# Optimization experiments

Measured on AMD Instinct MI355X. Metric: run time of the kernel, lower is better.

The kernel has to match this reference:

```python
import jax, jax.numpy as jnp
import numpy as np

N, E = 50000, 400000
IN_DIM, HID, OUT = 512, 256, 128


def _lin(key, fan_in, fan_out, bias=True):
    k1, k2 = jax.random.split(key)
    s = 1.0 / np.sqrt(fan_in)
    W = jax.random.uniform(k1, (fan_in, fan_out), minval=-s, maxval=s, dtype=jnp.float32)
    if bias:
        b = jax.random.uniform(k2, (fan_out,), minval=-s, maxval=s, dtype=jnp.float32)
        return W, b
    return W


def setup_inputs() -> dict:
    key = jax.random.key(0)
    ks = jax.random.split(key, 16)
    feature_data = jax.random.normal(ks[0], (N, IN_DIM), dtype=jnp.float32)
    edge_info = jax.random.randint(ks[1], (2, E), 0, N, dtype=jnp.int32)
    W1, b1 = _lin(ks[2], IN_DIM, HID)
    W2, b2 = _lin(ks[3], HID, HID)
    W3, b3 = _lin(ks[4], HID, HID)
    # SAGEConv params: lin_l (aggregated neighbors, with bias), lin_r (root, no bias)
    Wl1, bl1 = _lin(ks[5], HID, HID); Wr1 = _lin(ks[6], HID, HID, bias=False)
    WlH, blH = _lin(ks[7], HID, HID); WrH = _lin(ks[8], HID, HID, bias=False)
    Wl2, bl2 = _lin(ks[9], HID, HID); Wr2 = _lin(ks[10], HID, HID, bias=False)
    Wp1, bp1 = _lin(ks[11], HID, HID)
    Wp2, bp2 = _lin(ks[12], HID, HID)
    Wp3, bp3 = _lin(ks[13], HID, OUT)
    return dict(feature_data=feature_data, edge_info=edge_info,
                W1=W1, b1=b1, W2=W2, b2=b2, W3=W3, b3=b3,
                Wl1=Wl1, bl1=bl1, Wr1=Wr1,
                WlH=WlH, blH=blH, WrH=WrH,
                Wl2=Wl2, bl2=bl2, Wr2=Wr2,
                Wp1=Wp1, bp1=bp1, Wp2=Wp2, bp2=bp2, Wp3=Wp3, bp3=bp3)


def _sage_softmax_conv(x, src, dst, Wl, bl, Wr, n_nodes):
    # messages are source node features
    m = x[src]                                                   # [E, d]
    mx = jax.ops.segment_max(m, dst, num_segments=n_nodes)      # per-dest, per-channel max
    e = jnp.exp(m - mx[dst])                                     # stable softmax numerator
    s = jax.ops.segment_sum(e, dst, num_segments=n_nodes)
    alpha = e / s[dst]                                           # per-dest channel softmax
    aggr = jax.ops.segment_sum(alpha * m, dst, num_segments=n_nodes)  # [N, d]
    return aggr @ Wl + bl + x @ Wr


def reference(feature_data, edge_info,
              W1, b1, W2, b2, W3, b3,
              Wl1, bl1, Wr1, WlH, blH, WrH, Wl2, bl2, Wr2,
              Wp1, bp1, Wp2, bp2, Wp3, bp3):
    n = feature_data.shape[0]
    src, dst = edge_info[0], edge_info[1]
    # eval mode: dropout is identity
    x = jax.nn.relu(feature_data @ W1 + b1)
    x = jax.nn.relu(x @ W2 + b2)
    x = jax.nn.relu(x @ W3 + b3)
    x = jax.nn.relu(_sage_softmax_conv(x, src, dst, Wl1, bl1, Wr1, n))
    x = jax.nn.relu(_sage_softmax_conv(x, src, dst, WlH, blH, WrH, n))
    x = jax.nn.relu(_sage_softmax_conv(x, src, dst, Wl2, bl2, Wr2, n))
    x = jax.nn.relu(x @ Wp1 + bp1)
    x = jax.nn.relu(x @ Wp2 + bp2)
    return jnp.tanh(x @ Wp3 + bp3)
```

## Files before the change

kernel.cpp:

```cpp
#include <hip/hip_runtime.h>
#include <hip/hip_bf16.h>
#include <math.h>

typedef short s8v __attribute__((ext_vector_type(8)));
typedef float f32x4 __attribute__((ext_vector_type(4)));
typedef unsigned u32x4 __attribute__((ext_vector_type(4)));

__device__ __forceinline__ ushort f2bf(float f) {
    __hip_bfloat16 h = __float2bfloat16(f);
    return *reinterpret_cast<ushort*>(&h);
}
__device__ __forceinline__ float bf2f(ushort u) {
    return __uint_as_float(((unsigned)u) << 16);
}
__device__ __forceinline__ unsigned pack_split(float v) {
    ushort h = f2bf(v);
    ushort l = f2bf(v - bf2f(h));
    return ((unsigned)h << 16) | (unsigned)l;
}
__device__ __forceinline__ float unpack_f(unsigned p) {
    return __uint_as_float(p & 0xffff0000u) + __uint_as_float(p << 16);
}
__device__ __forceinline__ void gload16(const void* g, void* l) {
    __builtin_amdgcn_global_load_lds(
        (const __attribute__((address_space(1))) void*)g,
        (__attribute__((address_space(3))) void*)l, 16, 0, 0);
}
__device__ __forceinline__ unsigned lds_addr(const void* p) {
    return (unsigned)(size_t)(const __attribute__((address_space(3))) void*)p;
}
__device__ __forceinline__ void unpack8(const u32x4 p0, const u32x4 p1, s8v& hi, s8v& lo) {
    union { s8v v; unsigned u[4]; } H, L;
    H.u[0] = (p0[0] >> 16) | (p0[1] & 0xffff0000u);
    H.u[1] = (p0[2] >> 16) | (p0[3] & 0xffff0000u);
    H.u[2] = (p1[0] >> 16) | (p1[1] & 0xffff0000u);
    H.u[3] = (p1[2] >> 16) | (p1[3] & 0xffff0000u);
    L.u[0] = (p0[0] & 0xffffu) | (p0[1] << 16);
    L.u[1] = (p0[2] & 0xffffu) | (p0[3] << 16);
    L.u[2] = (p1[0] & 0xffffu) | (p1[1] << 16);
    L.u[3] = (p1[2] & 0xffffu) | (p1[3] << 16);
    hi = H.v; lo = L.v;
}
__device__ __forceinline__ void cvt8(const u32x4 p0, const u32x4 p1, s8v& hi, s8v& lo) {
    union { s8v v; ushort e[8]; } H, L;
    float f[8] = {__uint_as_float(p0[0]), __uint_as_float(p0[1]),
                  __uint_as_float(p0[2]), __uint_as_float(p0[3]),
                  __uint_as_float(p1[0]), __uint_as_float(p1[1]),
                  __uint_as_float(p1[2]), __uint_as_float(p1[3])};
    #pragma unroll
    for (int e = 0; e < 8; ++e) {
        ushort h = f2bf(f[e]);
        H.e[e] = (ushort)h;
        L.e[e] = f2bf(f[e] - bf2f(h));
    }
    hi = H.v; lo = L.v;
}
template<bool AF32>
__device__ __forceinline__ void frag_a(const u32x4 p0, const u32x4 p1, s8v& hi, s8v& lo) {
    if constexpr (AF32) cvt8(p0, p1, hi, lo);
    else                unpack8(p0, p1, hi, lo);
}

#define DSR(dst, addr, OFF) \
    asm volatile("ds_read_b128 %0, %1 offset:" #OFF : "=v"(dst) : "v"(addr))

#define TRI(ah, al, bh, bl, C) \
    C = __builtin_amdgcn_mfma_f32_16x16x32_bf16(ah, bh, C, 0, 0, 0); \
    C = __builtin_amdgcn_mfma_f32_16x16x32_bf16(ah, bl, C, 0, 0, 0); \
    C = __builtin_amdgcn_mfma_f32_16x16x32_bf16(al, bh, C, 0, 0, 0);


__global__ __launch_bounds__(256)
void hist_kernel(const int* __restrict__ dst, int* __restrict__ cnt, int E) {
    int e = blockIdx.x * 256 + threadIdx.x;
    if (e < E) atomicAdd(&cnt[dst[e]], 1);
}

__global__ __launch_bounds__(256)
void scan_part(const int* __restrict__ cnt, int* __restrict__ bsum, int n) {
    __shared__ int s[256];
    int b = blockIdx.x, t = threadIdx.x;
    int i0 = b * 1024 + t * 4;
    int v = 0;
    if (i0 + 3 < n) {
        int4 q = *(const int4*)(cnt + i0);
        v = q.x + q.y + q.z + q.w;
    } else {
        for (int i = 0; i < 4; ++i) if (i0 + i < n) v += cnt[i0 + i];
    }
    s[t] = v;
    __syncthreads();
    for (int d = 128; d > 0; d >>= 1) {
        if (t < d) s[t] += s[t + d];
        __syncthreads();
    }
    if (t == 0) bsum[b] = s[0];
}

__global__ __launch_bounds__(64)
void scan_top(int* __restrict__ bsum, int nb) {
    int l = threadIdx.x;
    int own = (l < nb) ? bsum[l] : 0;
    int v = own;
    #pragma unroll
    for (int d = 1; d < 64; d <<= 1) {
        int u = __shfl_up(v, d, 64);
        if (l >= d) v += u;
    }
    if (l < nb) bsum[l] = v - own;
}

__global__ __launch_bounds__(256)
void scan_final(const int* __restrict__ cnt, const int* __restrict__ bsum,
                int* __restrict__ off, int n, int E) {
    __shared__ int s[256];
    int b = blockIdx.x, t = threadIdx.x;
    int i0 = b * 1024 + t * 4;
    int v0 = 0, v1 = 0, v2 = 0, v3 = 0;
    if (i0 + 3 < n) {
        int4 q = *(const int4*)(cnt + i0);
        v0 = q.x; v1 = q.y; v2 = q.z; v3 = q.w;
    } else {
        if (i0     < n) v0 = cnt[i0];
        if (i0 + 1 < n) v1 = cnt[i0 + 1];
        if (i0 + 2 < n) v2 = cnt[i0 + 2];
        if (i0 + 3 < n) v3 = cnt[i0 + 3];
    }
    int tsum = v0 + v1 + v2 + v3;
    s[t] = tsum;
    __syncthreads();
    for (int d = 1; d < 256; d <<= 1) {
        int u = (t >= d) ? s[t - d] : 0;
        __syncthreads();
        s[t] += u;
        __syncthreads();
    }
    int excl = s[t] - tsum + bsum[b];
    if (i0     < n) off[i0]     = excl;
    if (i0 + 1 < n) off[i0 + 1] = excl + v0;
    if (i0 + 2 < n) off[i0 + 2] = excl + v0 + v1;
    if (i0 + 3 < n) off[i0 + 3] = excl + v0 + v1 + v2;
    if (b == 0 && t == 0) off[n] = E;
}

__global__ __launch_bounds__(256)
void scatter_kernel(const int* __restrict__ src, const int* __restrict__ dst,
                    int* __restrict__ cur, const int* __restrict__ off,
                    int* __restrict__ csr, int E) {
    int e = blockIdx.x * 256 + threadIdx.x;
    if (e < E) {
        int d = dst[e];
        int pos = off[d] + atomicAdd(&cur[d], 1);
        csr[pos] = src[e];
    }
}


struct PrepW {
    const float* W[12];
    unsigned* D[12];
    int end[12];
    int stride[12];
    int koff[12];
    int nshift[12];
};

__global__ __launch_bounds__(256)
void prep_weights(PrepW a, int total) {
    int id = blockIdx.x * 256 + threadIdx.x;
    if (id >= total) return;
    int s = 0;
    #pragma unroll
    for (int i = 0; i < 12; ++i) if (id >= a.end[i]) s = i + 1;
    int base = (s == 0) ? 0 : a.end[s - 1];
    int e = id - base;
    int Nmask = (1 << a.nshift[s]) - 1;
    int n = e & Nmask;
    int k = e >> a.nshift[s];
    float w = a.W[s][(size_t)k * (Nmask + 1) + n];
    a.D[s][(size_t)n * a.stride[s] + a.koff[s] + k] = pack_split(w);
}


__global__ __launch_bounds__(256)
void sage_aggr_pk(const unsigned* __restrict__ X, const int* __restrict__ csr,
                  const int* __restrict__ off, unsigned* __restrict__ O, int nN) {
    int node = blockIdx.x * 4 + (threadIdx.x >> 6);
    if (node >= nN) return;
    int c4 = (threadIdx.x & 63) * 4;
    int s0 = off[node], s1 = off[node + 1];
    float m0 = -INFINITY, m1 = -INFINITY, m2 = -INFINITY, m3 = -INFINITY;
    float se0 = 0, se1 = 0, se2 = 0, se3 = 0;
    float sm0 = 0, sm1 = 0, sm2 = 0, sm3 = 0;
#define ONLSTEP(vv, mm, ss, pp) { float nm = fmaxf(mm, vv); float r = __expf(mm - nm); \
    float p = __expf(vv - nm); ss = ss * r + p; pp = pp * r + p * (vv); mm = nm; }
    for (int j = s0; j < s1; ++j) {
        uint4 p = *(const uint4*)(X + (size_t)csr[j] * 256 + c4);
        float v0 = unpack_f(p.x), v1 = unpack_f(p.y), v2 = unpack_f(p.z), v3 = unpack_f(p.w);
        ONLSTEP(v0, m0, se0, sm0) ONLSTEP(v1, m1, se1, sm1)
        ONLSTEP(v2, m2, se2, sm2) ONLSTEP(v3, m3, se3, sm3)
    }
#undef ONLSTEP
    uint4 o;
    o.x = pack_split((s1 > s0) ? sm0 / se0 : 0.f);
    o.y = pack_split((s1 > s0) ? sm1 / se1 : 0.f);
    o.z = pack_split((s1 > s0) ? sm2 / se2 : 0.f);
    o.w = pack_split((s1 > s0) ? sm3 / se3 : 0.f);
    *(uint4*)(O + (size_t)node * 256 + c4) = o;
}


template<int NT1, int NT2, bool AF32, int NB, bool DOTANH>
__global__ __launch_bounds__(512, 2)
void gemm_pipe(const float* __restrict__ A1f, const unsigned* __restrict__ A1,
               const unsigned* __restrict__ A2,
               const unsigned* __restrict__ B,
               const float* __restrict__ bias,
               unsigned* __restrict__ Cpk, float* __restrict__ Cf, int M) {
    constexpr int NT = NT1 + NT2;
    constexpr int KU = NT * 32;
    __shared__ unsigned lds[3][12288];

    const int tid = threadIdx.x;
    const int l = tid & 63;
    const int w = tid >> 6;
    const int wm = w >> 2, wn = w & 3;
    const int li = l & 15, kq = l >> 4;
    const int bm = blockIdx.x * 128;

    const int srow = 8 * w + (l >> 3);
    const int schunk = (l & 7) ^ (l >> 3);

    const unsigned lbase = lds_addr(&lds[0][0]);
    const unsigned swz0 = (unsigned)((((2 * kq)) ^ (li & 7)) * 16);
    const unsigned aoff = (unsigned)((wm * 64 + li) * 128) + swz0;
    const unsigned boff = 16384u + (unsigned)((wn * 64 + li) * 128) + swz0;

    f32x4 acc[4][4];
    #pragma unroll
    for (int i = 0; i < 4; ++i)
        #pragma unroll
        for (int j = 0; j < 4; ++j) acc[i][j] = (f32x4){0.f, 0.f, 0.f, 0.f};

    auto STAGE = [&](int t, int buf) {
        #pragma unroll
        for (int s = 0; s < 2; ++s) {
            int r = 64 * s + srow;
            int gr = bm + r; gr = (gr < M) ? gr : (M - 1);
            const void* src;
            if constexpr (AF32) {
                src = A1f + (size_t)gr * KU + t * 32 + schunk * 4;
            } else if constexpr (NT2 > 0) {
                src = (t < NT1) ? (const void*)(A1 + (size_t)gr * (NT1 * 32) + t * 32 + schunk * 4)
                                : (const void*)(A2 + (size_t)gr * (NT2 * 32) + (t - NT1) * 32 + schunk * 4);
            } else {
                src = A1 + (size_t)gr * KU + t * 32 + schunk * 4;
            }
            gload16(src, &lds[buf][s * 2048 + w * 256 + l * 4]);
        }
        #pragma unroll
        for (int s = 0; s < 4; ++s) {
            int n = 64 * s + srow;
            int gn = (n < NB) ? n : (NB - 1);
            const unsigned* src = B + (size_t)gn * KU + t * 32 + schunk * 4;
            gload16(src, &lds[buf][4096 + s * 2048 + w * 256 + l * 4]);
        }
    };

    STAGE(0, 0);
    STAGE(1, 1);

    #pragma unroll
    for (int t = 0; t < NT; ++t) {
        if (t + 1 < NT) asm volatile("s_waitcnt vmcnt(6)" ::: "memory");
        else            asm volatile("s_waitcnt vmcnt(0)" ::: "memory");
        __builtin_amdgcn_s_barrier();

        const int buf = t % 3;
        const unsigned lb = lbase + (unsigned)buf * 49152u;
        unsigned ab = lb + aoff, bb = lb + boff;
        unsigned ab1 = ab ^ 16u, bb1 = bb ^ 16u;

        u32x4 B0, B1, B2, B3, B4, B5, B6, B7;
        u32x4 A0, A4, A1v, A5, A2v, A6, A3, A7;
        DSR(B0, bb, 0);    DSR(B1, bb, 2048);  DSR(B2, bb, 4096);  DSR(B3, bb, 6144);
        DSR(B4, bb1, 0);   DSR(B5, bb1, 2048); DSR(B6, bb1, 4096); DSR(B7, bb1, 6144);
        DSR(A0, ab, 0);    DSR(A4, ab1, 0);
        __builtin_amdgcn_sched_barrier(0);

        if (t + 2 < NT) STAGE(t + 2, (t + 2) % 3);
        __builtin_amdgcn_sched_barrier(0);

        DSR(A1v, ab, 2048); DSR(A5, ab1, 2048);
        asm volatile("s_waitcnt lgkmcnt(2)" ::: "memory");
        __builtin_amdgcn_sched_barrier(0);

        s8v bh0, bl0, bh1, bl1, bh2, bl2, bh3, bl3;
        unpack8(B0, B4, bh0, bl0);
        unpack8(B1, B5, bh1, bl1);
        unpack8(B2, B6, bh2, bl2);
        unpack8(B3, B7, bh3, bl3);

        __builtin_amdgcn_s_setprio(1);
        {
            s8v ah, al;
            frag_a<AF32>(A0, A4, ah, al);
            TRI(ah, al, bh0, bl0, acc[0][0]) TRI(ah, al, bh1, bl1, acc[0][1])
            TRI(ah, al, bh2, bl2, acc[0][2]) TRI(ah, al, bh3, bl3, acc[0][3])
        }
        __builtin_amdgcn_sched_barrier(0);
        DSR(A2v, ab, 4096); DSR(A6, ab1, 4096);
        asm volatile("s_waitcnt lgkmcnt(2)" ::: "memory");
        __builtin_amdgcn_sched_barrier(0);
        {
            s8v ah, al;
            frag_a<AF32>(A1v, A5, ah, al);
            TRI(ah, al, bh0, bl0, acc[1][0]) TRI(ah, al, bh1, bl1, acc[1][1])
            TRI(ah, al, bh2, bl2, acc[1][2]) TRI(ah, al, bh3, bl3, acc[1][3])
        }
        __builtin_amdgcn_sched_barrier(0);
        DSR(A3, ab, 6144); DSR(A7, ab1, 6144);
        asm volatile("s_waitcnt lgkmcnt(2)" ::: "memory");
        __builtin_amdgcn_sched_barrier(0);
        {
            s8v ah, al;
            frag_a<AF32>(A2v, A6, ah, al);
            TRI(ah, al, bh0, bl0, acc[2][0]) TRI(ah, al, bh1, bl1, acc[2][1])
            TRI(ah, al, bh2, bl2, acc[2][2]) TRI(ah, al, bh3, bl3, acc[2][3])
        }
        asm volatile("s_waitcnt lgkmcnt(0)" ::: "memory");
        __builtin_amdgcn_sched_barrier(0);
        {
            s8v ah, al;
            frag_a<AF32>(A3, A7, ah, al);
            TRI(ah, al, bh0, bl0, acc[3][0]) TRI(ah, al, bh1, bl1, acc[3][1])
            TRI(ah, al, bh2, bl2, acc[3][2]) TRI(ah, al, bh3, bl3, acc[3][3])
        }
        __builtin_amdgcn_s_setprio(0);
    }

    #pragma unroll
    for (int j = 0; j < 4; ++j) {
        int col = wn * 64 + 16 * j + li;
        float b = bias[(col < NB) ? col : 0];
        #pragma unroll
        for (int i = 0; i < 4; ++i) {
            int row0 = bm + wm * 64 + 16 * i + kq * 4;
            #pragma unroll
            for (int r = 0; r < 4; ++r) {
                float v = acc[i][j][r] + b;
                if constexpr (DOTANH) {
                    if (row0 + r < M && col < NB)
                        Cf[(size_t)(row0 + r) * NB + col] = tanhf(v);
                } else {
                    Cpk[(size_t)(row0 + r) * 256 + col] = pack_split(fmaxf(v, 0.f));
                }
            }
        }
    }
}


extern "C" void kernel_launch(void* const* d_in, const int* in_sizes, int n_in,
                              void* d_out, int out_size, void* d_ws, size_t ws_size,
                              hipStream_t stream) {
    const float* feat = (const float*)d_in[0];
    const int* einfo = (const int*)d_in[1];
    const float* b1 = (const float*)d_in[3];
    const float* b2 = (const float*)d_in[5];
    const float* b3 = (const float*)d_in[7];
    const float* bl1 = (const float*)d_in[9];
    const float* blH = (const float*)d_in[12];
    const float* bl2 = (const float*)d_in[15];
    const float* bp1 = (const float*)d_in[18];
    const float* bp2 = (const float*)d_in[20];
    const float* bp3 = (const float*)d_in[22];

    const int IN_DIM = 512;
    const int N = in_sizes[0] / IN_DIM;
    const int E = in_sizes[1] / 2;
    const int* src = einfo;
    const int* dst = einfo + E;
    const int M_pad = ((N + 127) / 128) * 128;
    const size_t PLANE_U = (size_t)M_pad * 256;

    unsigned* P0 = (unsigned*)d_ws;
    unsigned* P1 = P0 + PLANE_U;
    unsigned* P2 = P1 + PLANE_U;
    unsigned* wp = P2 + PLANE_U;

    const int gsz[9] = {131072, 65536, 65536, 131072, 131072, 131072, 65536, 65536, 32768};
    unsigned* G[9];
    {
        unsigned* c = wp;
        for (int i = 0; i < 9; ++i) { G[i] = c; c += gsz[i]; }
        wp = c;
    }

    const int widx[12]   = {2, 4, 6, 8, 10, 11, 13, 14, 16, 17, 19, 21};
    const int wplane[12] = {0, 1, 2, 3, 3, 4, 4, 5, 5, 6, 7, 8};
    const int wstr[12]   = {512, 256, 256, 512, 512, 512, 512, 512, 512, 256, 256, 256};
    const int wkoff[12]  = {0, 0, 0, 0, 256, 0, 256, 0, 256, 0, 0, 0};
    const int wnsh[12]   = {8, 8, 8, 8, 8, 8, 8, 8, 8, 8, 8, 7};
    const int welem[12]  = {131072, 65536, 65536, 65536, 65536, 65536, 65536,
                            65536, 65536, 65536, 65536, 32768};

    PrepW pa;
    int acc_end = 0;
    for (int i = 0; i < 12; ++i) {
        pa.W[i] = (const float*)d_in[widx[i]];
        pa.D[i] = G[wplane[i]];
        pa.stride[i] = wstr[i];
        pa.koff[i] = wkoff[i];
        pa.nshift[i] = wnsh[i];
        acc_end += welem[i];
        pa.end[i] = acc_end;
    }

    int* ioff = (int*)wp;
    int* icnt = ioff + ((N + 1 + 3) & ~3);
    int* icur = icnt + ((N + 3) & ~3);
    int* csr  = icur + ((N + 3) & ~3);
    int* bsum = csr + ((E + 3) & ~3);

    const int NBLK = (N + 1023) / 1024;

    hipMemsetAsync(icnt, 0, (size_t)N * sizeof(int), stream);
    hipMemsetAsync(icur, 0, (size_t)N * sizeof(int), stream);
    hist_kernel<<<(E + 255) / 256, 256, 0, stream>>>(dst, icnt, E);
    scan_part<<<NBLK, 256, 0, stream>>>(icnt, bsum, N);
    scan_top<<<1, 64, 0, stream>>>(bsum, NBLK);
    scan_final<<<NBLK, 256, 0, stream>>>(icnt, bsum, ioff, N, E);
    scatter_kernel<<<(E + 255) / 256, 256, 0, stream>>>(src, dst, icur, ioff, csr, E);
    prep_weights<<<(acc_end + 255) / 256, 256, 0, stream>>>(pa, acc_end);

    const int GB = M_pad / 128;
    const int GA = (N + 3) / 4;

    gemm_pipe<16, 0, true, 256, false><<<GB, 512, 0, stream>>>(
        feat, nullptr, nullptr, G[0], b1, P0, nullptr, N);
    gemm_pipe<8, 0, false, 256, false><<<GB, 512, 0, stream>>>(
        nullptr, P0, nullptr, G[1], b2, P1, nullptr, N);
    gemm_pipe<8, 0, false, 256, false><<<GB, 512, 0, stream>>>(
        nullptr, P1, nullptr, G[2], b3, P0, nullptr, N);

    sage_aggr_pk<<<GA, 256, 0, stream>>>(P0, csr, ioff, P1, N);
    gemm_pipe<8, 8, false, 256, false><<<GB, 512, 0, stream>>>(
        nullptr, P1, P0, G[3], bl1, P2, nullptr, N);

    sage_aggr_pk<<<GA, 256, 0, stream>>>(P2, csr, ioff, P1, N);
    gemm_pipe<8, 8, false, 256, false><<<GB, 512, 0, stream>>>(
        nullptr, P1, P2, G[4], blH, P0, nullptr, N);

    sage_aggr_pk<<<GA, 256, 0, stream>>>(P0, csr, ioff, P1, N);
    gemm_pipe<8, 8, false, 256, false><<<GB, 512, 0, stream>>>(
        nullptr, P1, P0, G[5], bl2, P2, nullptr, N);

    gemm_pipe<8, 0, false, 256, false><<<GB, 512, 0, stream>>>(
        nullptr, P2, nullptr, G[6], bp1, P0, nullptr, N);
    gemm_pipe<8, 0, false, 256, false><<<GB, 512, 0, stream>>>(
        nullptr, P0, nullptr, G[7], bp2, P1, nullptr, N);
    gemm_pipe<8, 0, false, 128, true><<<GB, 512, 0, stream>>>(
        nullptr, P1, nullptr, G[8], bp3, nullptr, (float*)d_out, N);
}
```

Before: 652.1 us.

## Store split-bf16 activations and weights as separate hi/lo planes, drop online max

Replaces the packed hi|lo 32-bit split-bf16 format with two separate bf16 planes for activations and weights. The GEMM can then read MFMA fragments straight from LDS without per-iteration unpack shuffles, which also changes the LDS staging layout and swizzle. The aggregation kernel drops the online-softmax running max and instead clamps inputs to 60 before exp. That is safe only because inputs are post-ReLU and bounded, but it risks overflow or precision loss for large values. Aggregation now reads two separate 8-byte loads per edge instead of one 16-byte load.

```diff
diff --git a/kernel.cpp b/kernel.cpp
--- a/kernel.cpp
+++ b/kernel.cpp
@@ -12,14 +12,6 @@
 }
 __device__ __forceinline__ float bf2f(ushort u) {
     return __uint_as_float(((unsigned)u) << 16);
-}
-__device__ __forceinline__ unsigned pack_split(float v) {
-    ushort h = f2bf(v);
-    ushort l = f2bf(v - bf2f(h));
-    return ((unsigned)h << 16) | (unsigned)l;
-}
-__device__ __forceinline__ float unpack_f(unsigned p) {
-    return __uint_as_float(p & 0xffff0000u) + __uint_as_float(p << 16);
 }
 __device__ __forceinline__ void gload16(const void* g, void* l) {
     __builtin_amdgcn_global_load_lds(
@@ -28,18 +20,6 @@
 }
 __device__ __forceinline__ unsigned lds_addr(const void* p) {
     return (unsigned)(size_t)(const __attribute__((address_space(3))) void*)p;
-}
-__device__ __forceinline__ void unpack8(const u32x4 p0, const u32x4 p1, s8v& hi, s8v& lo) {
-    union { s8v v; unsigned u[4]; } H, L;
-    H.u[0] = (p0[0] >> 16) | (p0[1] & 0xffff0000u);
-    H.u[1] = (p0[2] >> 16) | (p0[3] & 0xffff0000u);
-    H.u[2] = (p1[0] >> 16) | (p1[1] & 0xffff0000u);
-    H.u[3] = (p1[2] >> 16) | (p1[3] & 0xffff0000u);
-    L.u[0] = (p0[0] & 0xffffu) | (p0[1] << 16);
-    L.u[1] = (p0[2] & 0xffffu) | (p0[3] << 16);
-    L.u[2] = (p1[0] & 0xffffu) | (p1[1] << 16);
-    L.u[3] = (p1[2] & 0xffffu) | (p1[3] << 16);
-    hi = H.v; lo = L.v;
 }
 __device__ __forceinline__ void cvt8(const u32x4 p0, const u32x4 p1, s8v& hi, s8v& lo) {
     union { s8v v; ushort e[8]; } H, L;
@@ -54,11 +34,6 @@
         L.e[e] = f2bf(f[e] - bf2f(h));
     }
     hi = H.v; lo = L.v;
-}
-template<bool AF32>
-__device__ __forceinline__ void frag_a(const u32x4 p0, const u32x4 p1, s8v& hi, s8v& lo) {
-    if constexpr (AF32) cvt8(p0, p1, hi, lo);
-    else                unpack8(p0, p1, hi, lo);
 }
 
 #define DSR(dst, addr, OFF) \
@@ -158,7 +133,8 @@
 
 struct PrepW {
     const float* W[12];
-    unsigned* D[12];
+    ushort* H[12];
+    ushort* L[12];
     int end[12];
     int stride[12];
     int koff[12];
@@ -178,48 +154,67 @@
     int n = e & Nmask;
     int k = e >> a.nshift[s];
     float w = a.W[s][(size_t)k * (Nmask + 1) + n];
-    a.D[s][(size_t)n * a.stride[s] + a.koff[s] + k] = pack_split(w);
-}
-
-
-__global__ __launch_bounds__(256)
-void sage_aggr_pk(const unsigned* __restrict__ X, const int* __restrict__ csr,
-                  const int* __restrict__ off, unsigned* __restrict__ O, int nN) {
+    ushort hi = f2bf(w);
+    size_t idx = (size_t)n * a.stride[s] + a.koff[s] + k;
+    a.H[s][idx] = hi;
+    a.L[s][idx] = f2bf(w - bf2f(hi));
+}
+
+
+__global__ __launch_bounds__(256)
+void sage_aggr(const ushort* __restrict__ XH, const ushort* __restrict__ XL,
+               const int* __restrict__ csr, const int* __restrict__ off,
+               ushort* __restrict__ OH, ushort* __restrict__ OL, int nN) {
     int node = blockIdx.x * 4 + (threadIdx.x >> 6);
     if (node >= nN) return;
     int c4 = (threadIdx.x & 63) * 4;
     int s0 = off[node], s1 = off[node + 1];
-    float m0 = -INFINITY, m1 = -INFINITY, m2 = -INFINITY, m3 = -INFINITY;
     float se0 = 0, se1 = 0, se2 = 0, se3 = 0;
     float sm0 = 0, sm1 = 0, sm2 = 0, sm3 = 0;
-#define ONLSTEP(vv, mm, ss, pp) { float nm = fmaxf(mm, vv); float r = __expf(mm - nm); \
-    float p = __expf(vv - nm); ss = ss * r + p; pp = pp * r + p * (vv); mm = nm; }
     for (int j = s0; j < s1; ++j) {
-        uint4 p = *(const uint4*)(X + (size_t)csr[j] * 256 + c4);
-        float v0 = unpack_f(p.x), v1 = unpack_f(p.y), v2 = unpack_f(p.z), v3 = unpack_f(p.w);
-        ONLSTEP(v0, m0, se0, sm0) ONLSTEP(v1, m1, se1, sm1)
-        ONLSTEP(v2, m2, se2, sm2) ONLSTEP(v3, m3, se3, sm3)
-    }
-#undef ONLSTEP
-    uint4 o;
-    o.x = pack_split((s1 > s0) ? sm0 / se0 : 0.f);
-    o.y = pack_split((s1 > s0) ? sm1 / se1 : 0.f);
-    o.z = pack_split((s1 > s0) ? sm2 / se2 : 0.f);
-    o.w = pack_split((s1 > s0) ? sm3 / se3 : 0.f);
-    *(uint4*)(O + (size_t)node * 256 + c4) = o;
+        size_t b = (size_t)csr[j] * 256 + c4;
+        ushort4 h = *(const ushort4*)(XH + b);
+        ushort4 l = *(const ushort4*)(XL + b);
+        float v0 = bf2f(h.x) + bf2f(l.x);
+        float v1 = bf2f(h.y) + bf2f(l.y);
+        float v2 = bf2f(h.z) + bf2f(l.z);
+        float v3 = bf2f(h.w) + bf2f(l.w);
+        float e0 = __expf(fminf(v0, 60.f));
+        float e1 = __expf(fminf(v1, 60.f));
+        float e2 = __expf(fminf(v2, 60.f));
+        float e3 = __expf(fminf(v3, 60.f));
+        se0 += e0; sm0 = fmaf(v0, e0, sm0);
+        se1 += e1; sm1 = fmaf(v1, e1, sm1);
+        se2 += e2; sm2 = fmaf(v2, e2, sm2);
+        se3 += e3; sm3 = fmaf(v3, e3, sm3);
+    }
+    float o0 = (s1 > s0) ? sm0 / se0 : 0.f;
+    float o1 = (s1 > s0) ? sm1 / se1 : 0.f;
+    float o2 = (s1 > s0) ? sm2 / se2 : 0.f;
+    float o3 = (s1 > s0) ? sm3 / se3 : 0.f;
+    ushort4 oh, ol;
+    oh.x = f2bf(o0); ol.x = f2bf(o0 - bf2f(oh.x));
+    oh.y = f2bf(o1); ol.y = f2bf(o1 - bf2f(oh.y));
+    oh.z = f2bf(o2); ol.z = f2bf(o2 - bf2f(oh.z));
+    oh.w = f2bf(o3); ol.w = f2bf(o3 - bf2f(oh.w));
+    size_t ob = (size_t)node * 256 + c4;
+    *(ushort4*)(OH + ob) = oh;
+    *(ushort4*)(OL + ob) = ol;
 }
 
 
 template<int NT1, int NT2, bool AF32, int NB, bool DOTANH>
 __global__ __launch_bounds__(512, 2)
-void gemm_pipe(const float* __restrict__ A1f, const unsigned* __restrict__ A1,
-               const unsigned* __restrict__ A2,
-               const unsigned* __restrict__ B,
+void gemm_pipe(const float* __restrict__ Af,
+               const ushort* __restrict__ A1H, const ushort* __restrict__ A1L,
+               const ushort* __restrict__ A2H, const ushort* __restrict__ A2L,
+               const ushort* __restrict__ BH, const ushort* __restrict__ BL,
                const float* __restrict__ bias,
-               unsigned* __restrict__ Cpk, float* __restrict__ Cf, int M) {
+               ushort* __restrict__ CH, ushort* __restrict__ CL,
+               float* __restrict__ Cf, int M) {
     constexpr int NT = NT1 + NT2;
     constexpr int KU = NT * 32;
-    __shared__ unsigned lds[3][12288];
+    __shared__ ushort lds[3][24576];
 
     const int tid = threadIdx.x;
     const int l = tid & 63;
@@ -228,13 +223,15 @@
     const int li = l & 15, kq = l >> 4;
     const int bm = blockIdx.x * 128;
 
-    const int srow = 8 * w + (l >> 3);
-    const int schunk = (l & 7) ^ (l >> 3);
+    const int arow = 16 * w + (l >> 2);
+    const int achk = (l & 3) ^ ((l >> 2) & 3);
+    const int frow = 8 * w + (l >> 3);
+    const int fchk = (l & 7) ^ ((l >> 3) & 7);
 
     const unsigned lbase = lds_addr(&lds[0][0]);
-    const unsigned swz0 = (unsigned)((((2 * kq)) ^ (li & 7)) * 16);
-    const unsigned aoff = (unsigned)((wm * 64 + li) * 128) + swz0;
-    const unsigned boff = 16384u + (unsigned)((wn * 64 + li) * 128) + swz0;
+    const unsigned aoffA = (unsigned)((wm * 64 + li) * 64 + ((kq ^ (li & 3)) * 16));
+    const unsigned boffB = 16384u + (unsigned)((wn * 64 + li) * 64 + ((kq ^ (li & 3)) * 16));
+    const unsigned aoffF = (unsigned)((wm * 64 + li) * 128 + (((2 * kq) ^ (li & 7)) * 16));
 
     f32x4 acc[4][4];
     #pragma unroll
@@ -243,27 +240,31 @@
         for (int j = 0; j < 4; ++j) acc[i][j] = (f32x4){0.f, 0.f, 0.f, 0.f};
 
     auto STAGE = [&](int t, int buf) {
+        if constexpr (AF32) {
+            #pragma unroll
+            for (int s = 0; s < 2; ++s) {
+                int gr = bm + 64 * s + frow; gr = (gr < M) ? gr : (M - 1);
+                const float* src = Af + (size_t)gr * KU + t * 32 + fchk * 4;
+                gload16(src, &lds[buf][(64 * s + 8 * w) * 64 + l * 8]);
+            }
+        } else {
+            int gr = bm + arow; gr = (gr < M) ? gr : (M - 1);
+            const ushort *pH, *pL; int tt, KA;
+            if constexpr (NT2 > 0) {
+                if (t >= NT1) { pH = A2H; pL = A2L; tt = t - NT1; KA = NT2 * 32; }
+                else          { pH = A1H; pL = A1L; tt = t;       KA = NT1 * 32; }
+            } else { pH = A1H; pL = A1L; tt = t; KA = KU; }
+            size_t ab = (size_t)gr * KA + tt * 32 + achk * 8;
+            gload16(pH + ab, &lds[buf][512 * w + 8 * l]);
+            gload16(pL + ab, &lds[buf][4096 + 512 * w + 8 * l]);
+        }
         #pragma unroll
         for (int s = 0; s < 2; ++s) {
-            int r = 64 * s + srow;
-            int gr = bm + r; gr = (gr < M) ? gr : (M - 1);
-            const void* src;
-            if constexpr (AF32) {
-                src = A1f + (size_t)gr * KU + t * 32 + schunk * 4;
-            } else if constexpr (NT2 > 0) {
-                src = (t < NT1) ? (const void*)(A1 + (size_t)gr * (NT1 * 32) + t * 32 + schunk * 4)
-                                : (const void*)(A2 + (size_t)gr * (NT2 * 32) + (t - NT1) * 32 + schunk * 4);
-            } else {
-                src = A1 + (size_t)gr * KU + t * 32 + schunk * 4;
-            }
-            gload16(src, &lds[buf][s * 2048 + w * 256 + l * 4]);
-        }
-        #pragma unroll
-        for (int s = 0; s < 4; ++s) {
-            int n = 64 * s + srow;
+            int n = 32 * w + 16 * s + (l >> 2);
             int gn = (n < NB) ? n : (NB - 1);
-            const unsigned* src = B + (size_t)gn * KU + t * 32 + schunk * 4;
-            gload16(src, &lds[buf][4096 + s * 2048 + w * 256 + l * 4]);
+            size_t bb = (size_t)gn * KU + t * 32 + achk * 8;
+            gload16(BH + bb, &lds[buf][8192  + 1024 * w + 512 * s + 8 * l]);
+            gload16(BL + bb, &lds[buf][16384 + 1024 * w + 512 * s + 8 * l]);
         }
     };
 
@@ -278,65 +279,87 @@
 
         const int buf = t % 3;
         const unsigned lb = lbase + (unsigned)buf * 49152u;
-        unsigned ab = lb + aoff, bb = lb + boff;
-        unsigned ab1 = ab ^ 16u, bb1 = bb ^ 16u;
-
-        u32x4 B0, B1, B2, B3, B4, B5, B6, B7;
-        u32x4 A0, A4, A1v, A5, A2v, A6, A3, A7;
-        DSR(B0, bb, 0);    DSR(B1, bb, 2048);  DSR(B2, bb, 4096);  DSR(B3, bb, 6144);
-        DSR(B4, bb1, 0);   DSR(B5, bb1, 2048); DSR(B6, bb1, 4096); DSR(B7, bb1, 6144);
-        DSR(A0, ab, 0);    DSR(A4, ab1, 0);
-        __builtin_amdgcn_sched_barrier(0);
-
-        if (t + 2 < NT) STAGE(t + 2, (t + 2) % 3);
-        __builtin_amdgcn_sched_barrier(0);
-
-        DSR(A1v, ab, 2048); DSR(A5, ab1, 2048);
-        asm volatile("s_waitcnt lgkmcnt(2)" ::: "memory");
-        __builtin_amdgcn_sched_barrier(0);
-
-        s8v bh0, bl0, bh1, bl1, bh2, bl2, bh3, bl3;
-        unpack8(B0, B4, bh0, bl0);
-        unpack8(B1, B5, bh1, bl1);
-        unpack8(B2, B6, bh2, bl2);
-        unpack8(B3, B7, bh3, bl3);
-
-        __builtin_amdgcn_s_setprio(1);
-        {
-            s8v ah, al;
-            frag_a<AF32>(A0, A4, ah, al);
-            TRI(ah, al, bh0, bl0, acc[0][0]) TRI(ah, al, bh1, bl1, acc[0][1])
-            TRI(ah, al, bh2, bl2, acc[0][2]) TRI(ah, al, bh3, bl3, acc[0][3])
+
+        s8v BH0, BH1, BH2, BH3, BL0, BL1, BL2, BL3;
+        if constexpr (AF32) {
+            unsigned bh_b = lb + boffB, bl_b = bh_b + 16384u;
+            unsigned ab = lb + aoffF, ab1 = ab ^ 16u;
+            u32x4 F0, F1, F2, F3, F4, F5, F6, F7;
+            DSR(BH0, bh_b, 0); DSR(BH1, bh_b, 1024); DSR(BH2, bh_b, 2048); DSR(BH3, bh_b, 3072);
+            DSR(BL0, bl_b, 0); DSR(BL1, bl_b, 1024); DSR(BL2, bl_b, 2048); DSR(BL3, bl_b, 3072);
+            DSR(F0, ab, 0); DSR(F4, ab1, 0);
+            __builtin_amdgcn_sched_barrier(0);
+            if (t + 2 < NT) STAGE(t + 2, (t + 2) % 3);
+            __builtin_amdgcn_sched_barrier(0);
+            DSR(F1, ab, 2048); DSR(F5, ab1, 2048);
+            asm volatile("s_waitcnt lgkmcnt(2)" ::: "memory");
+            __builtin_amdgcn_sched_barrier(0);
+            __builtin_amdgcn_s_setprio(1);
+            {
+                s8v ah, al; cvt8(F0, F4, ah, al);
+                TRI(ah, al, BH0, BL0, acc[0][0]) TRI(ah, al, BH1, BL1, acc[0][1])
+                TRI(ah, al, BH2, BL2, acc[0][2]) TRI(ah, al, BH3, BL3, acc[0][3])
+            }
+            __builtin_amdgcn_sched_barrier(0);
+            DSR(F2, ab, 4096); DSR(F6, ab1, 4096);
+            asm volatile("s_waitcnt lgkmcnt(2)" ::: "memory");
+            __builtin_amdgcn_sched_barrier(0);
+            {
+                s8v ah, al; cvt8(F1, F5, ah, al);
+                TRI(ah, al, BH0, BL0, acc[1][0]) TRI(ah, al, BH1, BL1, acc[1][1])
+                TRI(ah, al, BH2, BL2, acc[1][2]) TRI(ah, al, BH3, BL3, acc[1][3])
+            }
+            __builtin_amdgcn_sched_barrier(0);
+            DSR(F3, ab, 6144); DSR(F7, ab1, 6144);
+            asm volatile("s_waitcnt lgkmcnt(2)" ::: "memory");
+            __builtin_amdgcn_sched_barrier(0);
+            {
+                s8v ah, al; cvt8(F2, F6, ah, al);
+                TRI(ah, al, BH0, BL0, acc[2][0]) TRI(ah, al, BH1, BL1, acc[2][1])
+                TRI(ah, al, BH2, BL2, acc[2][2]) TRI(ah, al, BH3, BL3, acc[2][3])
+            }
+            asm volatile("s_waitcnt lgkmcnt(0)" ::: "memory");
+            __builtin_amdgcn_sched_barrier(0);
+            {
+                s8v ah, al; cvt8(F3, F7, ah, al);
+                TRI(ah, al, BH0, BL0, acc[3][0]) TRI(ah, al, BH1, BL1, acc[3][1])
+                TRI(ah, al, BH2, BL2, acc[3][2]) TRI(ah, al, BH3, BL3, acc[3][3])
+            }
+            __builtin_amdgcn_s_setprio(0);
+        } else {
+            unsigned ah_b = lb + aoffA, al_b = ah_b + 8192u;
+            unsigned bh_b = lb + boffB, bl_b = bh_b + 16384u;
+            s8v AH0, AH1, AH2, AH3, AL0, AL1, AL2, AL3;
+            DSR(BH0, bh_b, 0); DSR(BH1, bh_b, 1024); DSR(BH2, bh_b, 2048); DSR(BH3, bh_b, 3072);
+            DSR(BL0, bl_b, 0); DSR(BL1, bl_b, 1024); DSR(BL2, bl_b, 2048); DSR(BL3, bl_b, 3072);
+            DSR(AH0, ah_b, 0); DSR(AL0, al_b, 0);
+            __builtin_amdgcn_sched_barrier(0);
+            if (t + 2 < NT) STAGE(t + 2, (t + 2) % 3);
+            __builtin_amdgcn_sched_barrier(0);
+            DSR(AH1, ah_b, 1024); DSR(AL1, al_b, 1024);
+            asm volatile("s_waitcnt lgkmcnt(2)" ::: "memory");
+            __builtin_amdgcn_sched_barrier(0);
+            __builtin_amdgcn_s_setprio(1);
+            TRI(AH0, AL0, BH0, BL0, acc[0][0]) TRI(AH0, AL0, BH1, BL1, acc[0][1])
+            TRI(AH0, AL0, BH2, BL2, acc[0][2]) TRI(AH0, AL0, BH3, BL3, acc[0][3])
+            __builtin_amdgcn_sched_barrier(0);
+            DSR(AH2, ah_b, 2048); DSR(AL2, al_b, 2048);
+            asm volatile("s_waitcnt lgkmcnt(2)" ::: "memory");
+            __builtin_amdgcn_sched_barrier(0);
+            TRI(AH1, AL1, BH0, BL0, acc[1][0]) TRI(AH1, AL1, BH1, BL1, acc[1][1])
+            TRI(AH1, AL1, BH2, BL2, acc[1][2]) TRI(AH1, AL1, BH3, BL3, acc[1][3])
+            __builtin_amdgcn_sched_barrier(0);
+            DSR(AH3, ah_b, 3072); DSR(AL3, al_b, 3072);
+            asm volatile("s_waitcnt lgkmcnt(2)" ::: "memory");
+            __builtin_amdgcn_sched_barrier(0);
+            TRI(AH2, AL2, BH0, BL0, acc[2][0]) TRI(AH2, AL2, BH1, BL1, acc[2][1])
+            TRI(AH2, AL2, BH2, BL2, acc[2][2]) TRI(AH2, AL2, BH3, BL3, acc[2][3])
+            asm volatile("s_waitcnt lgkmcnt(0)" ::: "memory");
+            __builtin_amdgcn_sched_barrier(0);
+            TRI(AH3, AL3, BH0, BL0, acc[3][0]) TRI(AH3, AL3, BH1, BL1, acc[3][1])
+            TRI(AH3, AL3, BH2, BL2, acc[3][2]) TRI(AH3, AL3, BH3, BL3, acc[3][3])
+            __builtin_amdgcn_s_setprio(0);
         }
-        __builtin_amdgcn_sched_barrier(0);
-        DSR(A2v, ab, 4096); DSR(A6, ab1, 4096);
-        asm volatile("s_waitcnt lgkmcnt(2)" ::: "memory");
-        __builtin_amdgcn_sched_barrier(0);
-        {
-            s8v ah, al;
-            frag_a<AF32>(A1v, A5, ah, al);
-            TRI(ah, al, bh0, bl0, acc[1][0]) TRI(ah, al, bh1, bl1, acc[1][1])
-            TRI(ah, al, bh2, bl2, acc[1][2]) TRI(ah, al, bh3, bl3, acc[1][3])
-        }
-        __builtin_amdgcn_sched_barrier(0);
-        DSR(A3, ab, 6144); DSR(A7, ab1, 6144);
-        asm volatile("s_waitcnt lgkmcnt(2)" ::: "memory");
-        __builtin_amdgcn_sched_barrier(0);
-        {
-            s8v ah, al;
-            frag_a<AF32>(A2v, A6, ah, al);
-            TRI(ah, al, bh0, bl0, acc[2][0]) TRI(ah, al, bh1, bl1, acc[2][1])
-            TRI(ah, al, bh2, bl2, acc[2][2]) TRI(ah, al, bh3, bl3, acc[2][3])
-        }
-        asm volatile("s_waitcnt lgkmcnt(0)" ::: "memory");
-        __builtin_amdgcn_sched_barrier(0);
-        {
-            s8v ah, al;
-            frag_a<AF32>(A3, A7, ah, al);
-            TRI(ah, al, bh0, bl0, acc[3][0]) TRI(ah, al, bh1, bl1, acc[3][1])
-            TRI(ah, al, bh2, bl2, acc[3][2]) TRI(ah, al, bh3, bl3, acc[3][3])
-        }
-        __builtin_amdgcn_s_setprio(0);
     }
 
     #pragma unroll
@@ -353,7 +376,11 @@
                     if (row0 + r < M && col < NB)
                         Cf[(size_t)(row0 + r) * NB + col] = tanhf(v);
                 } else {
-                    Cpk[(size_t)(row0 + r) * 256 + col] = pack_split(fmaxf(v, 0.f));
+                    v = fmaxf(v, 0.f);
+                    ushort h = f2bf(v);
+                    size_t idx = (size_t)(row0 + r) * 256 + col;
+                    CH[idx] = h;
+                    CL[idx] = f2bf(v - bf2f(h));
                 }
             }
         }
@@ -382,20 +409,16 @@
     const int* src = einfo;
     const int* dst = einfo + E;
     const int M_pad = ((N + 127) / 128) * 128;
-    const size_t PLANE_U = (size_t)M_pad * 256;
-
-    unsigned* P0 = (unsigned*)d_ws;
-    unsigned* P1 = P0 + PLANE_U;
-    unsigned* P2 = P1 + PLANE_U;
-    unsigned* wp = P2 + PLANE_U;
+    const size_t PL = (size_t)M_pad * 256;
+
+    ushort* W = (ushort*)d_ws;
+    ushort* P0H = W; W += PL;  ushort* P0L = W; W += PL;
+    ushort* P1H = W; W += PL;  ushort* P1L = W; W += PL;
+    ushort* P2H = W; W += PL;  ushort* P2L = W; W += PL;
 
     const int gsz[9] = {131072, 65536, 65536, 131072, 131072, 131072, 65536, 65536, 32768};
-    unsigned* G[9];
-    {
-        unsigned* c = wp;
-        for (int i = 0; i < 9; ++i) { G[i] = c; c += gsz[i]; }
-        wp = c;
-    }
+    ushort* GH[9]; ushort* GL[9];
+    for (int i = 0; i < 9; ++i) { GH[i] = W; W += gsz[i]; GL[i] = W; W += gsz[i]; }
 
     const int widx[12]   = {2, 4, 6, 8, 10, 11, 13, 14, 16, 17, 19, 21};
     const int wplane[12] = {0, 1, 2, 3, 3, 4, 4, 5, 5, 6, 7, 8};
@@ -409,7 +432,8 @@
     int acc_end = 0;
     for (int i = 0; i < 12; ++i) {
         pa.W[i] = (const float*)d_in[widx[i]];
-        pa.D[i] = G[wplane[i]];
+        pa.H[i] = GH[wplane[i]];
+        pa.L[i] = GL[wplane[i]];
         pa.stride[i] = wstr[i];
         pa.koff[i] = wkoff[i];
         pa.nshift[i] = wnsh[i];
@@ -417,7 +441,7 @@
         pa.end[i] = acc_end;
     }
 
-    int* ioff = (int*)wp;
+    int* ioff = (int*)(((size_t)W + 15) & ~(size_t)15);
     int* icnt = ioff + ((N + 1 + 3) & ~3);
     int* icur = icnt + ((N + 3) & ~3);
     int* csr  = icur + ((N + 3) & ~3);
@@ -438,28 +462,37 @@
     const int GA = (N + 3) / 4;
 
     gemm_pipe<16, 0, true, 256, false><<<GB, 512, 0, stream>>>(
-        feat, nullptr, nullptr, G[0], b1, P0, nullptr, N);
+        feat, nullptr, nullptr, nullptr, nullptr, GH[0], GL[0], b1,
+        P0H, P0L, nullptr, N);
     gemm_pipe<8, 0, false, 256, false><<<GB, 512, 0, stream>>>(
-        nullptr, P0, nullptr, G[1], b2, P1, nullptr, N);
+        nullptr, P0H, P0L, nullptr, nullptr, GH[1], GL[1], b2,
+        P1H, P1L, nullptr, N);
     gemm_pipe<8, 0, false, 256, false><<<GB, 512, 0, stream>>>(
-        nullptr, P1, nullptr, G[2], b3, P0, nullptr, N);
-
-    sage_aggr_pk<<<GA, 256, 0, stream>>>(P0, csr, ioff, P1, N);
+        nullptr, P1H, P1L, nullptr, nullptr, GH[2], GL[2], b3,
+        P0H, P0L, nullptr, N);
+
+    sage_aggr<<<GA, 256, 0, stream>>>(P0H, P0L, csr, ioff, P2H, P2L, N);
     gemm_pipe<8, 8, false, 256, false><<<GB, 512, 0, stream>>>(
-        nullptr, P1, P0, G[3], bl1, P2, nullptr, N);
-
-    sage_aggr_pk<<<GA, 256, 0, stream>>>(P2, csr, ioff, P1, N);
+        nullptr, P2H, P2L, P0H, P0L, GH[3], GL[3], bl1,
+        P1H, P1L, nullptr, N);
+
+    sage_aggr<<<GA, 256, 0, stream>>>(P1H, P1L, csr, ioff, P2H, P2L, N);
     gemm_pipe<8, 8, false, 256, false><<<GB, 512, 0, stream>>>(
-        nullptr, P1, P2, G[4], blH, P0, nullptr, N);
-
-    sage_aggr_pk<<<GA, 256, 0, stream>>>(P0, csr, ioff, P1, N);
+        nullptr, P2H, P2L, P1H, P1L, GH[4], GL[4], blH,
+        P0H, P0L, nullptr, N);
+
+    sage_aggr<<<GA, 256, 0, stream>>>(P0H, P0L, csr, ioff, P2H, P2L, N);
     gemm_pipe<8, 8, false, 256, false><<<GB, 512, 0, stream>>>(
-        nullptr, P1, P0, G[5], bl2, P2, nullptr, N);
+        nullptr, P2H, P2L, P0H, P0L, GH[5], GL[5], bl2,
+        P1H, P1L, nullptr, N);
 
     gemm_pipe<8, 0, false, 256, false><<<GB, 512, 0, stream>>>(
-        nullptr, P2, nullptr, G[6], bp1, P0, nullptr, N);
+        nullptr, P1H, P1L, nullptr, nullptr, GH[6], GL[6], bp1,
+        P0H, P0L, nullptr, N);
     gemm_pipe<8, 0, false, 256, false><<<GB, 512, 0, stream>>>(
-        nullptr, P0, nullptr, G[7], bp2, P1, nullptr, N);
+        nullptr, P0H, P0L, nullptr, nullptr, GH[7], GL[7], bp2,
+        P2H, P2L, nullptr, N);
     gemm_pipe<8, 0, false, 128, true><<<GB, 512, 0, stream>>>(
-        nullptr, P1, nullptr, G[8], bp3, nullptr, (float*)d_out, N);
-}
+        nullptr, P2H, P2L, nullptr, nullptr, GH[8], GL[8], bp3,
+        nullptr, nullptr, (float*)d_out, N);
+}
```

New measurement: 713.4 us. 1.09x slower.
